# Kernel tuning notes

Measured on AMD Instinct MI355X. Metric: run time of the kernel, lower is better.

The kernel has to match this reference:

```python
import jax, jax.numpy as jnp
import numpy as np

B, S, D_IN = 16, 4096, 1024
H, HD = 8, 64            # num_heads, head_dim
V = H * HD               # value_dim = 512
F_OUT = 120              # forecast_horizon
EPS = 1e-5


def _rotate(x):
    # theta_shift in the source ignores sin/cos: stack((-x2, x1)) and flatten
    x1 = x[..., 0::2]
    x2 = x[..., 1::2]
    return jnp.stack((-x2, x1), axis=-1).reshape(x.shape)


def setup_inputs() -> dict:
    key = jax.random.key(0)
    kx, kq, kk, kv, ko, _ = jax.random.split(key, 6)
    return {
        "x": jax.random.normal(kx, (B, S, D_IN), dtype=jnp.float32),
        "Wq": jax.random.normal(kq, (V, D_IN), dtype=jnp.float32) * 0.02,
        "Wk": jax.random.normal(kk, (V, D_IN), dtype=jnp.float32) * 0.02,
        "Wv": jax.random.normal(kv, (V, D_IN), dtype=jnp.float32) * 0.02,
        "Wout": jax.random.normal(ko, (F_OUT, V), dtype=jnp.float32) * 0.02,
        "gamma": jnp.ones((V,), dtype=jnp.float32),  # RMSNorm weight
    }


def reference(x, Wq, Wk, Wv, Wout, gamma):
    b, s, _ = x.shape
    scaling = HD ** -0.5
    q = (x @ Wq.T) * scaling          # [B,S,V]
    k = (x @ Wk.T) * scaling
    v = (x @ Wv.T).reshape(b, H, s, HD)   # raw view reinterpretation (as in torch)
    qr = _rotate(q).reshape(b, H, s, HD)  # raw view, matches torch .view
    kr = _rotate(k).reshape(b, H, s, HD)
    # recurrent_forward with incremental_state=None:
    # kv = 0.9*0 + 0.1*(kr*v); output = sum_s(qr*kv); scale = S
    kv = 0.1 * (kr * v)
    out = jnp.sum(qr * kv, axis=2) / jnp.float32(s)  # [B,H,HD]
    out = out.reshape(b, H * HD)                      # [B,V]
    # RMSNorm
    rms = out * jax.lax.rsqrt(jnp.mean(out * out, axis=-1, keepdims=True) + EPS) * gamma
    g = jax.nn.gelu(rms, approximate=False)  # torch F.gelu default = exact erf
    return g @ Wout.T                         # [B, forecast_horizon]
```

## Files before the change

kernel.cpp:

```cpp
#include <hip/hip_runtime.h>
#include <hip/hip_bf16.h>
#include <math.h>

#define B_   16
#define S_   4096
#define DIN  1024
#define V_   512
#define FOUT 120

typedef __attribute__((ext_vector_type(8))) short bf16x8;
typedef __attribute__((ext_vector_type(4))) float f32x4;

#define AS1 __attribute__((address_space(1)))
#define AS3 __attribute__((address_space(3)))

__device__ const float CSCALE = 0.1f / (64.0f * 4096.0f);
__device__ const float EPSF = 1e-5f;

__device__ inline void gl2lds16(const void* g, void* l) {
  __builtin_amdgcn_global_load_lds((const AS1 unsigned int*)g,
                                   (AS3 unsigned int*)l, 16, 0, 0);
}

__device__ inline unsigned short f2b(float f) {
  unsigned u = __builtin_bit_cast(unsigned, f);
  unsigned r = (u + 0x7FFFu + ((u >> 16) & 1u)) >> 16;
  return (unsigned short)r;
}

__device__ inline bf16x8 pack8(float4 a, float4 b) {
  bf16x8 r;
  r[0] = (short)f2b(a.x); r[1] = (short)f2b(a.y);
  r[2] = (short)f2b(a.z); r[3] = (short)f2b(a.w);
  r[4] = (short)f2b(b.x); r[5] = (short)f2b(b.y);
  r[6] = (short)f2b(b.z); r[7] = (short)f2b(b.w);
  return r;
}

__global__ void msr_convw(const float* __restrict__ Wq, const float* __restrict__ Wk,
                          const float* __restrict__ Wv, unsigned short* __restrict__ Wt) {
  int e = blockIdx.x * 256 + threadIdx.x;
  int l = e & 63;
  int f = (e >> 6) % 24;
  int ck = (e >> 6) / 24;
  int k = ck & 31;
  int ct = ck >> 5;
  int nf = f / 3, g = f % 3;
  const float* W = (g == 0) ? Wq : (g == 1) ? Wk : Wv;
  int ch = ct * 128 + nf * 16 + (l & 15);
  const float* src = W + (size_t)ch * DIN + k * 32 + (l >> 4) * 8;
  float4 a = *(const float4*)src;
  float4 b = *(const float4*)(src + 4);
  *(bf16x8*)(Wt + (size_t)e * 8) = pack8(a, b);
}

__global__ __launch_bounds__(256) void msr_convx(const float* __restrict__ x,
                                                 unsigned short* __restrict__ Xb) {
  const size_t stride = (size_t)gridDim.x * 256;
  for (size_t i = blockIdx.x * 256ull + threadIdx.x; i < 8388608ull; i += stride) {
    const float* src = x + i * 8;
    float4 a = *(const float4*)src;
    float4 b = *(const float4*)(src + 4);
    *(bf16x8*)(Xb + i * 8) = pack8(a, b);
  }
}

#define WAITVM5  asm volatile("s_waitcnt vmcnt(5)" ::: "memory")
#define WAITVM3  asm volatile("s_waitcnt vmcnt(3)" ::: "memory")
#define WAITVM0  asm volatile("s_waitcnt vmcnt(0)" ::: "memory")
#define WAITLGKM asm volatile("s_waitcnt lgkmcnt(0)" ::: "memory")
#define BARRIER  { asm volatile("" ::: "memory"); __builtin_amdgcn_s_barrier(); asm volatile("" ::: "memory"); }

template <bool DIRECT>
__global__ __launch_bounds__(512, 2) void msr_main(
    const float* __restrict__ x, const unsigned short* __restrict__ Xb,
    const unsigned short* __restrict__ Wt, float* __restrict__ outacc) {
  const int bid = blockIdx.x;
  const int xcd = bid & 7;
  const int j = bid >> 3;
  const int ct = j & 3;
  const int rt = xcd * 32 + (j >> 2);
  const int r0 = rt << 8;

  __shared__ __align__(16) unsigned char smem_[122880];

  const int t = threadIdx.x;
  const int w = t >> 6, lane = t & 63;
  const int l16 = lane * 16;
  const int w3 = w * 3;
  const int ctk = ct * 32;
  const int amb = (w >> 2) * 8192;
  const int bread = 16384 + 6 * (w & 3) * 1024 + l16;

  const unsigned short* srcA0 =
      Xb + (size_t)(r0 + w * 16 + (lane & 15)) * DIN + ((lane >> 4) << 3);
  const unsigned short* srcA1 = srcA0 + (size_t)128 * DIN;
  const float* pXf = x + (size_t)(r0 + w * 16 + (lane & 15)) * DIN + ((lane >> 4) << 3);

  f32x4 acc[3][8][2];
#pragma unroll
  for (int g = 0; g < 3; ++g)
#pragma unroll
    for (int m = 0; m < 8; ++m)
#pragma unroll
      for (int n = 0; n < 2; ++n) acc[g][m][n] = (f32x4){0.f, 0.f, 0.f, 0.f};

#define STAGE(KK, SB) { \
  unsigned char* _sb = smem_ + (SB) * 40960; \
  if constexpr (DIRECT) { \
    gl2lds16(srcA0 + (size_t)(KK) * 32, _sb + w * 1024); \
    gl2lds16(srcA1 + (size_t)(KK) * 32, _sb + (8 + w) * 1024); \
  } else { \
    const float* _p0 = pXf + (size_t)(KK) * 32; \
    const float* _p1 = _p0 + (size_t)128 * DIN; \
    *(bf16x8*)(_sb + (w * 64 + lane) * 16) = \
        pack8(*(const float4*)_p0, *(const float4*)(_p0 + 4)); \
    *(bf16x8*)(_sb + ((8 + w) * 64 + lane) * 16) = \
        pack8(*(const float4*)_p1, *(const float4*)(_p1 + 4)); \
  } \
  _Pragma("unroll") for (int i = 0; i < 3; ++i) \
    gl2lds16(Wt + ((size_t)(ctk + (KK)) * 24 + w3 + i) * 512 + (size_t)lane * 8, \
             _sb + 16384 + (w3 + i) * 1024); }

#define COMPUTE(KB) { \
  const unsigned char* _kb = smem_ + (KB) * 40960; \
  bf16x8 _bfr[6]; \
  _Pragma("unroll") for (int i = 0; i < 6; ++i) \
    _bfr[i] = *(const bf16x8*)(_kb + bread + i * 1024); \
  __builtin_amdgcn_s_setprio(1); \
  _Pragma("unroll") for (int m = 0; m < 8; ++m) { \
    bf16x8 _afr = *(const bf16x8*)(_kb + amb + m * 1024 + l16); \
    _Pragma("unroll") for (int g = 0; g < 3; ++g) { \
      acc[g][m][0] = __builtin_amdgcn_mfma_f32_16x16x32_bf16(_afr, _bfr[g],     acc[g][m][0], 0, 0, 0); \
      acc[g][m][1] = __builtin_amdgcn_mfma_f32_16x16x32_bf16(_afr, _bfr[3 + g], acc[g][m][1], 0, 0, 0); \
    } \
  } \
  __builtin_amdgcn_s_setprio(0); }

#define STEP(KB, SB, KK, DOSTAGE, VMD, VMF) { \
  if (DOSTAGE) { STAGE((KK) + 2, SB); } \
  COMPUTE(KB); \
  if constexpr (DIRECT) { VMD; } else { WAITLGKM; VMF; } \
  BARRIER; }

  STAGE(0, 0);
  STAGE(1, 1);
  if constexpr (DIRECT) { WAITVM5; } else { WAITLGKM; WAITVM3; }
  BARRIER;

#pragma unroll 1
  for (int i = 0; i < 10; ++i) {
    const int k3 = i * 3;
    STEP(0, 2, k3,     1, WAITVM5, WAITVM3);
    STEP(1, 0, k3 + 1, 1, WAITVM5, WAITVM3);
    STEP(2, 1, k3 + 2, 1, WAITVM5, WAITVM3);
  }
  STEP(0, 0, 30, 0, WAITVM0, WAITVM0);
  COMPUTE(1);
#undef STEP
#undef COMPUTE
#undef STAGE

  float pd0 = 0.f, pd1 = 0.f;
#pragma unroll
  for (int m = 0; m < 8; ++m)
#pragma unroll
    for (int r = 0; r < 4; ++r) {
      float qk0 = acc[0][m][0][r] * acc[1][m][0][r];
      float qk1 = acc[0][m][1][r] * acc[1][m][1][r];
      pd0 += __shfl_xor(qk0, 1, 64) * acc[2][m][0][r];
      pd1 += __shfl_xor(qk1, 1, 64) * acc[2][m][1][r];
    }
  pd0 += __shfl_xor(pd0, 16, 64); pd0 += __shfl_xor(pd0, 32, 64);
  pd1 += __shfl_xor(pd1, 16, 64); pd1 += __shfl_xor(pd1, 32, 64);

  if (lane < 16) {
    float* dst = &outacc[((rt >> 1) << 6) + (w & 1) * 32 + lane];
    atomicAdd(dst, pd0);
    atomicAdd(dst + 16, pd1);
  }
}

__global__ __launch_bounds__(256) void msr_finish(
    const float* __restrict__ outacc, const float* __restrict__ gamma,
    const float* __restrict__ Wout, float* __restrict__ y) {
  const int b = blockIdx.x;
  const int t = threadIdx.x;
  __shared__ float g[V_];
  __shared__ float wsum[4];

  float v0 = outacc[b * V_ + t] * CSCALE;
  float v1 = outacc[b * V_ + 256 + t] * CSCALE;
  float ss = v0 * v0 + v1 * v1;
#pragma unroll
  for (int o = 32; o > 0; o >>= 1) ss += __shfl_down(ss, o, 64);
  if ((t & 63) == 0) wsum[t >> 6] = ss;
  __syncthreads();
  float tot = wsum[0] + wsum[1] + wsum[2] + wsum[3];
  float rs = rsqrtf(tot * (1.0f / (float)V_) + EPSF);

  float r0v = v0 * rs * gamma[t];
  float r1v = v1 * rs * gamma[t + 256];
  g[t]       = 0.5f * r0v * (1.0f + erff(r0v * 0.70710678118654752f));
  g[t + 256] = 0.5f * r1v * (1.0f + erff(r1v * 0.70710678118654752f));
  __syncthreads();

  if (t < FOUT) {
    const float* wr = Wout + (size_t)t * V_;
    float acc = 0.f;
#pragma unroll 4
    for (int c = 0; c < V_; c += 4) {
      float4 w4 = *(const float4*)(wr + c);
      acc += g[c] * w4.x + g[c + 1] * w4.y + g[c + 2] * w4.z + g[c + 3] * w4.w;
    }
    y[b * FOUT + t] = acc;
  }
}

extern "C" void kernel_launch(void* const* d_in, const int* in_sizes, int n_in,
                              void* d_out, int out_size, void* d_ws, size_t ws_size,
                              hipStream_t stream) {
  const float* x     = (const float*)d_in[0];
  const float* Wq    = (const float*)d_in[1];
  const float* Wk    = (const float*)d_in[2];
  const float* Wv    = (const float*)d_in[3];
  const float* Wout  = (const float*)d_in[4];
  const float* gamma = (const float*)d_in[5];

  float* outacc = (float*)d_ws;
  unsigned short* Wt = (unsigned short*)((char*)d_ws + 32768);
  unsigned short* Xb = (unsigned short*)((char*)d_ws + 32768 + 3145728);
  float* y = (float*)d_out;

  const size_t need = 32768ull + 3145728ull + 134217728ull;

  msr_convw<<<768, 256, 0, stream>>>(Wq, Wk, Wv, Wt);
  hipMemsetAsync(outacc, 0, B_ * V_ * sizeof(float), stream);

  if (ws_size >= need) {
    msr_convx<<<2048, 256, 0, stream>>>(x, Xb);
    msr_main<true><<<1024, 512, 0, stream>>>(x, Xb, Wt, outacc);
  } else {
    msr_main<false><<<1024, 512, 0, stream>>>(x, Xb, Wt, outacc);
  }
  msr_finish<<<B_, 256, 0, stream>>>(outacc, gamma, Wout, y);
}
```

Before: 255.3 us.

## Load weight fragments straight into registers and shrink the LDS footprint

The weight (B) fragments no longer go through LDS. Each wave now loads them straight from global memory into a pair of register buffers, prefetching one k-step ahead, while only the activation tiles stay triple-buffered in LDS. This cuts shared memory per block from 120 KB to 48 KB, so two blocks can fit on a CU as the launch bounds ask, and it drops the LDS reads for B. Wait counts and a scheduling barrier are adjusted to match the new count of outstanding memory ops. In exchange, waves that share the same B fragments now each fetch them from global/L2, and register pressure rises with the double-buffered fragments.

```diff
diff --git a/kernel.cpp b/kernel.cpp
--- a/kernel.cpp
+++ b/kernel.cpp
@@ -65,10 +65,11 @@
   }
 }
 
-#define WAITVM5  asm volatile("s_waitcnt vmcnt(5)" ::: "memory")
-#define WAITVM3  asm volatile("s_waitcnt vmcnt(3)" ::: "memory")
+#define WAITVM8  asm volatile("s_waitcnt vmcnt(8)" ::: "memory")
+#define WAITVM6  asm volatile("s_waitcnt vmcnt(6)" ::: "memory")
 #define WAITVM0  asm volatile("s_waitcnt vmcnt(0)" ::: "memory")
 #define WAITLGKM asm volatile("s_waitcnt lgkmcnt(0)" ::: "memory")
+#define SCHEDB   __builtin_amdgcn_sched_barrier(0)
 #define BARRIER  { asm volatile("" ::: "memory"); __builtin_amdgcn_s_barrier(); asm volatile("" ::: "memory"); }
 
 template <bool DIRECT>
@@ -82,15 +83,15 @@
   const int rt = xcd * 32 + (j >> 2);
   const int r0 = rt << 8;
 
-  __shared__ __align__(16) unsigned char smem_[122880];
+  __shared__ __align__(16) unsigned char smem_[49152];
 
   const int t = threadIdx.x;
   const int w = t >> 6, lane = t & 63;
   const int l16 = lane * 16;
-  const int w3 = w * 3;
-  const int ctk = ct * 32;
   const int amb = (w >> 2) * 8192;
-  const int bread = 16384 + 6 * (w & 3) * 1024 + l16;
+
+  const unsigned short* pB =
+      Wt + (((size_t)ct * 32) * 24 + 6 * (w & 3)) * 512 + (size_t)lane * 8;
 
   const unsigned short* srcA0 =
       Xb + (size_t)(r0 + w * 16 + (lane & 15)) * DIN + ((lane >> 4) << 3);
@@ -105,8 +106,10 @@
 #pragma unroll
       for (int n = 0; n < 2; ++n) acc[g][m][n] = (f32x4){0.f, 0.f, 0.f, 0.f};
 
-#define STAGE(KK, SB) { \
-  unsigned char* _sb = smem_ + (SB) * 40960; \
+  bf16x8 bE[6], bO[6];
+
+#define STAGEA(KK, SB) { \
+  unsigned char* _sb = smem_ + (SB) * 16384; \
   if constexpr (DIRECT) { \
     gl2lds16(srcA0 + (size_t)(KK) * 32, _sb + w * 1024); \
     gl2lds16(srcA1 + (size_t)(KK) * 32, _sb + (8 + w) * 1024); \
@@ -117,49 +120,59 @@
         pack8(*(const float4*)_p0, *(const float4*)(_p0 + 4)); \
     *(bf16x8*)(_sb + ((8 + w) * 64 + lane) * 16) = \
         pack8(*(const float4*)_p1, *(const float4*)(_p1 + 4)); \
-  } \
-  _Pragma("unroll") for (int i = 0; i < 3; ++i) \
-    gl2lds16(Wt + ((size_t)(ctk + (KK)) * 24 + w3 + i) * 512 + (size_t)lane * 8, \
-             _sb + 16384 + (w3 + i) * 1024); }
-
-#define COMPUTE(KB) { \
-  const unsigned char* _kb = smem_ + (KB) * 40960; \
-  bf16x8 _bfr[6]; \
+  } }
+
+#define LOADB(dst, KK) { \
+  const unsigned short* _pb = pB + (size_t)(KK) * 12288; \
   _Pragma("unroll") for (int i = 0; i < 6; ++i) \
-    _bfr[i] = *(const bf16x8*)(_kb + bread + i * 1024); \
+    dst[i] = *(const bf16x8*)(_pb + i * 512); }
+
+#define COMPUTE(KB, BF) { \
+  const unsigned char* _kb = smem_ + (KB) * 16384; \
   __builtin_amdgcn_s_setprio(1); \
   _Pragma("unroll") for (int m = 0; m < 8; ++m) { \
     bf16x8 _afr = *(const bf16x8*)(_kb + amb + m * 1024 + l16); \
     _Pragma("unroll") for (int g = 0; g < 3; ++g) { \
-      acc[g][m][0] = __builtin_amdgcn_mfma_f32_16x16x32_bf16(_afr, _bfr[g],     acc[g][m][0], 0, 0, 0); \
-      acc[g][m][1] = __builtin_amdgcn_mfma_f32_16x16x32_bf16(_afr, _bfr[3 + g], acc[g][m][1], 0, 0, 0); \
+      acc[g][m][0] = __builtin_amdgcn_mfma_f32_16x16x32_bf16(_afr, BF[g],     acc[g][m][0], 0, 0, 0); \
+      acc[g][m][1] = __builtin_amdgcn_mfma_f32_16x16x32_bf16(_afr, BF[3 + g], acc[g][m][1], 0, 0, 0); \
     } \
   } \
   __builtin_amdgcn_s_setprio(0); }
 
-#define STEP(KB, SB, KK, DOSTAGE, VMD, VMF) { \
-  if (DOSTAGE) { STAGE((KK) + 2, SB); } \
-  COMPUTE(KB); \
-  if constexpr (DIRECT) { VMD; } else { WAITLGKM; VMF; } \
+#define STEP(KB, SB, KK, CUR, NXT) { \
+  LOADB(NXT, (KK) + 1); \
+  STAGEA((KK) + 2, SB); \
+  SCHEDB; \
+  COMPUTE(KB, CUR); \
+  if constexpr (DIRECT) { WAITVM8; } else { WAITLGKM; } \
   BARRIER; }
 
-  STAGE(0, 0);
-  STAGE(1, 1);
-  if constexpr (DIRECT) { WAITVM5; } else { WAITLGKM; WAITVM3; }
+  STAGEA(0, 0);
+  STAGEA(1, 1);
+  LOADB(bE, 0);
+  if constexpr (DIRECT) { WAITVM8; } else { WAITLGKM; }
   BARRIER;
 
 #pragma unroll 1
-  for (int i = 0; i < 10; ++i) {
-    const int k3 = i * 3;
-    STEP(0, 2, k3,     1, WAITVM5, WAITVM3);
-    STEP(1, 0, k3 + 1, 1, WAITVM5, WAITVM3);
-    STEP(2, 1, k3 + 2, 1, WAITVM5, WAITVM3);
-  }
-  STEP(0, 0, 30, 0, WAITVM0, WAITVM0);
-  COMPUTE(1);
+  for (int i = 0; i < 5; ++i) {
+    const int k6 = i * 6;
+    STEP(0, 2, k6,     bE, bO);
+    STEP(1, 0, k6 + 1, bO, bE);
+    STEP(2, 1, k6 + 2, bE, bO);
+    STEP(0, 2, k6 + 3, bO, bE);
+    STEP(1, 0, k6 + 4, bE, bO);
+    STEP(2, 1, k6 + 5, bO, bE);
+  }
+  LOADB(bO, 31);
+  SCHEDB;
+  COMPUTE(0, bE);
+  if constexpr (DIRECT) { WAITVM6; } else { WAITLGKM; }
+  BARRIER;
+  COMPUTE(1, bO);
 #undef STEP
 #undef COMPUTE
-#undef STAGE
+#undef LOADB
+#undef STAGEA
 
   float pd0 = 0.f, pd1 = 0.f;
 #pragma unroll
```

Measured after the change: 844.8 us. +230.8%, slower.

## Fuse fp32-to-bf16 x conversion into main GEMM with register-prefetched loads

Applied to the files above, without the earlier changes.

Removes the separate pass that converted x to bf16 in workspace and instead loads fp32 x directly in the main kernel. The fp32 loads for step k+2 go into registers a step ahead and are packed into LDS one step later, so global latency overlaps with the MFMA work. This drops a full read and write of the 128MB bf16 copy plus a kernel launch. In exchange it adds register pressure (two 4-float4 sets per thread), VALU packing work inside the loop, and a changed waitcnt and scheduling-barrier structure.

```diff
diff --git a/kernel.cpp b/kernel.cpp
--- a/kernel.cpp
+++ b/kernel.cpp
@@ -54,27 +54,15 @@
   *(bf16x8*)(Wt + (size_t)e * 8) = pack8(a, b);
 }
 
-__global__ __launch_bounds__(256) void msr_convx(const float* __restrict__ x,
-                                                 unsigned short* __restrict__ Xb) {
-  const size_t stride = (size_t)gridDim.x * 256;
-  for (size_t i = blockIdx.x * 256ull + threadIdx.x; i < 8388608ull; i += stride) {
-    const float* src = x + i * 8;
-    float4 a = *(const float4*)src;
-    float4 b = *(const float4*)(src + 4);
-    *(bf16x8*)(Xb + i * 8) = pack8(a, b);
-  }
-}
-
-#define WAITVM5  asm volatile("s_waitcnt vmcnt(5)" ::: "memory")
-#define WAITVM3  asm volatile("s_waitcnt vmcnt(3)" ::: "memory")
+#define WAITVM7  asm volatile("s_waitcnt vmcnt(7)" ::: "memory")
 #define WAITVM0  asm volatile("s_waitcnt vmcnt(0)" ::: "memory")
 #define WAITLGKM asm volatile("s_waitcnt lgkmcnt(0)" ::: "memory")
+#define SCHEDB   __builtin_amdgcn_sched_barrier(0)
 #define BARRIER  { asm volatile("" ::: "memory"); __builtin_amdgcn_s_barrier(); asm volatile("" ::: "memory"); }
 
-template <bool DIRECT>
 __global__ __launch_bounds__(512, 2) void msr_main(
-    const float* __restrict__ x, const unsigned short* __restrict__ Xb,
-    const unsigned short* __restrict__ Wt, float* __restrict__ outacc) {
+    const float* __restrict__ x, const unsigned short* __restrict__ Wt,
+    float* __restrict__ outacc) {
   const int bid = blockIdx.x;
   const int xcd = bid & 7;
   const int j = bid >> 3;
@@ -91,10 +79,9 @@
   const int ctk = ct * 32;
   const int amb = (w >> 2) * 8192;
   const int bread = 16384 + 6 * (w & 3) * 1024 + l16;
-
-  const unsigned short* srcA0 =
-      Xb + (size_t)(r0 + w * 16 + (lane & 15)) * DIN + ((lane >> 4) << 3);
-  const unsigned short* srcA1 = srcA0 + (size_t)128 * DIN;
+  const int aw0 = (w * 64 + lane) * 16;
+  const int aw1 = ((8 + w) * 64 + lane) * 16;
+
   const float* pXf = x + (size_t)(r0 + w * 16 + (lane & 15)) * DIN + ((lane >> 4) << 3);
 
   f32x4 acc[3][8][2];
@@ -105,22 +92,24 @@
 #pragma unroll
       for (int n = 0; n < 2; ++n) acc[g][m][n] = (f32x4){0.f, 0.f, 0.f, 0.f};
 
-#define STAGE(KK, SB) { \
+  float4 xE[4], xO[4];
+
+#define STAGEB(KK, SB) { \
   unsigned char* _sb = smem_ + (SB) * 40960; \
-  if constexpr (DIRECT) { \
-    gl2lds16(srcA0 + (size_t)(KK) * 32, _sb + w * 1024); \
-    gl2lds16(srcA1 + (size_t)(KK) * 32, _sb + (8 + w) * 1024); \
-  } else { \
-    const float* _p0 = pXf + (size_t)(KK) * 32; \
-    const float* _p1 = _p0 + (size_t)128 * DIN; \
-    *(bf16x8*)(_sb + (w * 64 + lane) * 16) = \
-        pack8(*(const float4*)_p0, *(const float4*)(_p0 + 4)); \
-    *(bf16x8*)(_sb + ((8 + w) * 64 + lane) * 16) = \
-        pack8(*(const float4*)_p1, *(const float4*)(_p1 + 4)); \
-  } \
   _Pragma("unroll") for (int i = 0; i < 3; ++i) \
     gl2lds16(Wt + ((size_t)(ctk + (KK)) * 24 + w3 + i) * 512 + (size_t)lane * 8, \
              _sb + 16384 + (w3 + i) * 1024); }
+
+#define LOADX(NX, KK) { \
+  const float* _p0 = pXf + (size_t)(KK) * 32; \
+  const float* _p1 = _p0 + (size_t)128 * DIN; \
+  NX[0] = *(const float4*)_p0; NX[1] = *(const float4*)(_p0 + 4); \
+  NX[2] = *(const float4*)_p1; NX[3] = *(const float4*)(_p1 + 4); }
+
+#define WRITEA(CX, AB) { \
+  unsigned char* _ab = smem_ + (AB) * 40960; \
+  *(bf16x8*)(_ab + aw0) = pack8(CX[0], CX[1]); \
+  *(bf16x8*)(_ab + aw1) = pack8(CX[2], CX[3]); }
 
 #define COMPUTE(KB) { \
   const unsigned char* _kb = smem_ + (KB) * 40960; \
@@ -137,29 +126,45 @@
   } \
   __builtin_amdgcn_s_setprio(0); }
 
-#define STEP(KB, SB, KK, DOSTAGE, VMD, VMF) { \
-  if (DOSTAGE) { STAGE((KK) + 2, SB); } \
+#define STEP(KB, SB, AB, KK, CX, NX) { \
+  STAGEB((KK) + 2, SB); \
+  LOADX(NX, (KK) + 2); \
+  WRITEA(CX, AB); \
+  SCHEDB; \
   COMPUTE(KB); \
-  if constexpr (DIRECT) { VMD; } else { WAITLGKM; VMF; } \
+  WAITVM7; WAITLGKM; \
   BARRIER; }
 
-  STAGE(0, 0);
-  STAGE(1, 1);
-  if constexpr (DIRECT) { WAITVM5; } else { WAITLGKM; WAITVM3; }
+  LOADX(xE, 0);
+  STAGEB(0, 0);
+  STAGEB(1, 1);
+  WRITEA(xE, 0);
+  LOADX(xO, 1);
+  WAITVM7;
+  WAITLGKM;
   BARRIER;
 
 #pragma unroll 1
-  for (int i = 0; i < 10; ++i) {
-    const int k3 = i * 3;
-    STEP(0, 2, k3,     1, WAITVM5, WAITVM3);
-    STEP(1, 0, k3 + 1, 1, WAITVM5, WAITVM3);
-    STEP(2, 1, k3 + 2, 1, WAITVM5, WAITVM3);
+  for (int i = 0; i < 5; ++i) {
+    const int k6 = i * 6;
+    STEP(0, 2, 1, k6,     xO, xE);
+    STEP(1, 0, 2, k6 + 1, xE, xO);
+    STEP(2, 1, 0, k6 + 2, xO, xE);
+    STEP(0, 2, 1, k6 + 3, xE, xO);
+    STEP(1, 0, 2, k6 + 4, xO, xE);
+    STEP(2, 1, 0, k6 + 5, xE, xO);
   }
-  STEP(0, 0, 30, 0, WAITVM0, WAITVM0);
+  WRITEA(xO, 1);
+  SCHEDB;
+  COMPUTE(0);
+  WAITVM0; WAITLGKM;
+  BARRIER;
   COMPUTE(1);
 #undef STEP
 #undef COMPUTE
-#undef STAGE
+#undef WRITEA
+#undef LOADX
+#undef STAGEB
 
   float pd0 = 0.f, pd1 = 0.f;
 #pragma unroll
@@ -229,19 +234,10 @@
 
   float* outacc = (float*)d_ws;
   unsigned short* Wt = (unsigned short*)((char*)d_ws + 32768);
-  unsigned short* Xb = (unsigned short*)((char*)d_ws + 32768 + 3145728);
   float* y = (float*)d_out;
-
-  const size_t need = 32768ull + 3145728ull + 134217728ull;
 
   msr_convw<<<768, 256, 0, stream>>>(Wq, Wk, Wv, Wt);
   hipMemsetAsync(outacc, 0, B_ * V_ * sizeof(float), stream);
-
-  if (ws_size >= need) {
-    msr_convx<<<2048, 256, 0, stream>>>(x, Xb);
-    msr_main<true><<<1024, 512, 0, stream>>>(x, Xb, Wt, outacc);
-  } else {
-    msr_main<false><<<1024, 512, 0, stream>>>(x, Xb, Wt, outacc);
-  }
+  msr_main<<<1024, 512, 0, stream>>>(x, Wt, outacc);
   msr_finish<<<B_, 256, 0, stream>>>(outacc, gamma, Wout, y);
 }
```

After: 872.5 us. 3.42x slower.
